# Optimization experiments

Measured on AMD Instinct MI355X. Metric: run time of the kernel, lower is better.

Reference implementation:

```python
import jax, jax.numpy as jnp
import numpy as np

N_NODES, N_EDGES, N_FEAT, DIM, HEADS, N_PRED, N_CLASS, N_STEPS = 10000, 160000, 64, 64, 4, 2, 16, 4


def setup_inputs() -> dict:
    key = jax.random.key(0)
    ks = jax.random.split(key, 16)
    def lin(k, fi, fo):
        return jax.random.normal(k, (fi, fo), jnp.float32) / np.sqrt(fi)
    return {
        "x": jax.random.normal(ks[0], (N_NODES, N_FEAT), jnp.float32),
        "edge_index": jax.random.randint(ks[1], (2, N_EDGES), 0, N_NODES, jnp.int64),
        "enc_W": lin(ks[2], N_FEAT, DIM), "enc_b": jnp.zeros((DIM,), jnp.float32),
        "gat_Wl": lin(ks[3], DIM, HEADS * DIM), "gat_bl": jnp.zeros((HEADS * DIM,), jnp.float32),
        "gat_Wr": lin(ks[4], DIM, HEADS * DIM), "gat_br": jnp.zeros((HEADS * DIM,), jnp.float32),
        "gat_att": jax.random.normal(ks[5], (HEADS, DIM), jnp.float32) / np.sqrt(DIM),
        "gat_bias": jnp.zeros((HEADS * DIM,), jnp.float32),
        "W1": lin(ks[6], HEADS * DIM, DIM), "b1": jnp.zeros((DIM,), jnp.float32),
        "W2": lin(ks[7], DIM, DIM), "b2": jnp.zeros((DIM,), jnp.float32),
        "act_W": lin(ks[8], DIM, 1), "act_b": jnp.zeros((1,), jnp.float32),
        "dec_W": jax.random.normal(ks[9], (N_PRED, DIM, N_CLASS), jnp.float32) / np.sqrt(DIM),
        "dec_b": jnp.zeros((N_PRED, N_CLASS), jnp.float32),
        "num_steps": N_STEPS,
    }


def reference(x, edge_index, enc_W, enc_b, gat_Wl, gat_bl, gat_Wr, gat_br,
              gat_att, gat_bias, W1, b1, W2, b2, act_W, act_b, dec_W, dec_b, num_steps):
    N = x.shape[0]
    H, C = gat_att.shape  # heads, per-head channels
    # PyG GATv2Conv adds self-loops by default
    loops = jnp.arange(N, dtype=edge_index.dtype)
    src = jnp.concatenate([edge_index[0], loops])
    dst = jnp.concatenate([edge_index[1], loops])

    h0 = x @ enc_W + enc_b  # encoder

    def step(carry, _):
        h, total, final = carry
        # GATv2: per-edge score on lin_l(src) + lin_r(dst)
        xl = (h @ gat_Wl + gat_bl).reshape(N, H, C)
        xr = (h @ gat_Wr + gat_br).reshape(N, H, C)
        e = jax.nn.leaky_relu(xl[src] + xr[dst], 0.2)          # [E, H, C]
        logits = jnp.einsum('ehc,hc->eh', e, gat_att)           # [E, H]
        m = jax.ops.segment_max(logits, dst, num_segments=N)    # segment softmax over dst
        ex = jnp.exp(logits - m[dst])
        denom = jax.ops.segment_sum(ex, dst, num_segments=N)
        alpha = ex / (denom[dst] + 1e-16)
        agg = jax.ops.segment_sum(xl[src] * alpha[:, :, None], dst, num_segments=N)
        g = agg.reshape(N, H * C) + gat_bias                    # concat heads + bias
        hn = jax.nn.relu(g @ W1 + b1) @ W2 + b2                 # process2 MLP
        # ACT halting: weighted accumulation, deltas clipped so weights sum to <= 1
        term = jax.nn.sigmoid(hn @ act_W + act_b)               # [N, 1]
        new_total = jnp.minimum(total + term, 1.0)
        delta = jnp.minimum(term, new_total - total)
        return (hn, total + delta, final + delta * hn), None

    carry0 = (h0, jnp.zeros((N, 1), x.dtype), jnp.zeros((N, h0.shape[1]), x.dtype))
    (_, _, final), _ = jax.lax.scan(step, carry0, None, length=num_steps)

    logits = jnp.einsum('nd,pdc->pnc', final, dec_W) + dec_b[:, None, :]
    return jax.nn.log_softmax(logits, axis=-1)  # [num_predictions, N, num_classes]
```

## Files before the change

kernel.cpp:

```cpp
#include <hip/hip_runtime.h>
#include <hip/hip_bf16.h>
#include <hip/hip_fp16.h>

#define N_NODES 10000
#define N_EDGES 160000
#define N_E2    (N_EDGES + N_NODES)
#define DIM     64
#define HD      256
#define N_PRED  2
#define N_CLASS 16
#define N_STEPS 4

typedef __hip_bfloat16 bf16;
__device__ __forceinline__ float b2f(bf16 v) { return __bfloat162float(v); }
__device__ __forceinline__ int clampn(int v) { return v < 0 ? 0 : (v >= N_NODES ? N_NODES - 1 : v); }

typedef _Float16 h2_t __attribute__((ext_vector_type(2)));

__device__ __forceinline__ float dot2(unsigned int a, unsigned int b, float c) {
#if __has_builtin(__builtin_amdgcn_fdot2)
    h2_t av, bv;
    __builtin_memcpy(&av, &a, 4);
    __builtin_memcpy(&bv, &b, 4);
    return __builtin_amdgcn_fdot2(av, bv, c, false);
#else
    __half2 ah = *(__half2*)&a, bh = *(__half2*)&b;
    float2 af = __half22float2(ah), bf = __half22float2(bh);
    return c + af.x * bf.x + af.y * bf.y;
#endif
}

struct ConvTable {
    const void* src[17];
    int start[18];
};

__device__ __forceinline__ float loadf(const void* p, int idx, int isbf16) {
    return isbf16 ? b2f(((const bf16*)p)[idx]) : ((const float*)p)[idx];
}

__global__ void detect_kernel(const unsigned int* __restrict__ e32,
                              const unsigned short* __restrict__ x16,
                              int* __restrict__ flags,
                              int* __restrict__ deg, int* __restrict__ cursor) {
    __shared__ int ce, cf;
    if (threadIdx.x == 0) { ce = 0; cf = 0; }
    __syncthreads();
    int le = 0;
    for (int i = threadIdx.x; i < 2048; i += 256)
        le += (e32[2 * i + 1] != 0u) ? 1 : 0;
    int lf = 0;
    for (int i = threadIdx.x; i < 1024; i += 256) {
        unsigned short u = x16[2 * i];
        int ex = (u >> 7) & 0xFF;
        lf += (u == 0 || (ex >= 114 && ex <= 141)) ? 1 : 0;
    }
    atomicAdd(&ce, le);
    atomicAdd(&cf, lf);
    for (int i = threadIdx.x; i < N_NODES; i += 256) { deg[i] = 0; cursor[i] = 0; }
    __syncthreads();
    if (threadIdx.x == 0) {
        flags[0] = (ce < 1024) ? 1 : 0;
        flags[1] = (cf >= 512) ? 1 : 0;
    }
}

struct PreArgs {
    ConvTable tab;
    const void* Wl_raw; const void* Wr_raw; const void* W1_raw; const void* W2_raw;
    const int* edges;
    int cb, pb;
};

__global__ void pre_kernel(PreArgs a, const int* __restrict__ flags,
                           float* __restrict__ xf, __half* __restrict__ wp,
                           int* __restrict__ deg) {
    const int b = blockIdx.x, t = threadIdx.x;
    const int isb = flags[1];
    if (b < a.cb) {
        int i = b * 256 + t;
        if (i >= a.tab.start[17]) return;
        int j = 0;
        #pragma unroll
        for (int k = 1; k < 17; ++k) j += (i >= a.tab.start[k]) ? 1 : 0;
        xf[i] = loadf(a.tab.src[j], i - a.tab.start[j], isb);
    } else if (b < a.cb + a.pb) {
        int i = (b - a.cb) * 256 + t;
        if (i >= 26624) return;
        const void* base; int width, loc;
        if (i < 8192)       { loc = i;         base = a.Wl_raw; width = 256; }
        else if (i < 16384) { loc = i - 8192;  base = a.Wr_raw; width = 256; }
        else if (i < 24576) { loc = i - 16384; base = a.W1_raw; width = 64; }
        else                { loc = i - 24576; base = a.W2_raw; width = 64; }
        int k2 = loc / width, c = loc % width;
        wp[2 * i]     = __float2half(loadf(base, (2 * k2) * width + c, isb));
        wp[2 * i + 1] = __float2half(loadf(base, (2 * k2 + 1) * width + c, isb));
    } else {
        int e = (b - a.cb - a.pb) * 256 + t;
        if (e >= N_E2) return;
        int i64 = flags[0];
        int dst;
        if (e < N_EDGES) dst = clampn(i64 ? a.edges[2 * (N_EDGES + e)] : a.edges[N_EDGES + e]);
        else             dst = e - N_EDGES;
        atomicAdd(&deg[dst], 1);
    }
}

__global__ void scan_kernel(const int* __restrict__ deg, int* __restrict__ off) {
    __shared__ int partial[1024];
    const int tid = threadIdx.x;
    const int per = (N_NODES + 1023) / 1024;
    int local[16];
    int base = tid * per;
    int s = 0;
    for (int i = 0; i < per; ++i) {
        int v = (base + i < N_NODES) ? deg[base + i] : 0;
        local[i] = s;
        s += v;
    }
    partial[tid] = s;
    __syncthreads();
    for (int d = 1; d < 1024; d <<= 1) {
        int t = (tid >= d) ? partial[tid - d] : 0;
        __syncthreads();
        partial[tid] += t;
        __syncthreads();
    }
    int offset = (tid > 0) ? partial[tid - 1] : 0;
    for (int i = 0; i < per; ++i)
        if (base + i < N_NODES) off[base + i] = offset + local[i];
    if (tid == 1023) off[N_NODES] = partial[1023];
}

struct SEArgs {
    const int* edges;
    const int* off;
    int* cursor;
    int* csr_src;
    const float* xf;
    int sX, sEncW, sEncB, sWl, sBl, sWr, sBr;
    __half* xlh;
    float* xr;
    float* act_tot;
    float* final_;
    int sb;
};

__global__ __launch_bounds__(256) void scatter_enc_kernel(SEArgs a, const int* __restrict__ flags) {
    const int b = blockIdx.x, t = threadIdx.x;
    if (b < a.sb) {
        int e = b * 256 + t;
        if (e >= N_E2) return;
        int i64 = flags[0];
        int src, dst;
        if (e < N_EDGES) {
            src = clampn(i64 ? a.edges[2 * e] : a.edges[e]);
            dst = clampn(i64 ? a.edges[2 * (N_EDGES + e)] : a.edges[N_EDGES + e]);
        } else { src = dst = e - N_EDGES; }
        int pos = a.off[dst] + atomicAdd(&a.cursor[dst], 1);
        a.csr_src[pos] = src;
        return;
    }
    __shared__ float xs[8][DIM];
    __shared__ float h0[8][DIM];
    const int pp = t >> 6, d = t & 63;
    const int n0 = (b - a.sb) * 8;
    const float* Xf   = a.xf + a.sX;
    const float* encW = a.xf + a.sEncW;
    const float* encB = a.xf + a.sEncB;
    const float* Wl   = a.xf + a.sWl;
    const float* bl   = a.xf + a.sBl;
    const float* Wr   = a.xf + a.sWr;
    const float* br   = a.xf + a.sBr;
    ((float*)xs)[t]       = Xf[n0 * DIM + t];
    ((float*)xs)[t + 256] = Xf[n0 * DIM + t + 256];
    a.final_[(size_t)n0 * DIM + t]       = 0.f;
    a.final_[(size_t)n0 * DIM + t + 256] = 0.f;
    if (t < 8) a.act_tot[n0 + t] = 0.f;
    __syncthreads();
    float ah0 = encB[d], ah1 = encB[d];
    for (int k = 0; k < DIM; ++k) {
        float wv = encW[k * DIM + d];
        ah0 += xs[pp][k] * wv;
        ah1 += xs[pp + 4][k] * wv;
    }
    h0[pp][d]     = ah0;
    h0[pp + 4][d] = ah1;
    __syncthreads();
    float al[8] = {0,0,0,0,0,0,0,0}, ar[8] = {0,0,0,0,0,0,0,0};
    for (int k = 0; k < DIM; ++k) {
        float wl = Wl[k * HD + t], wr = Wr[k * HD + t];
        #pragma unroll
        for (int j = 0; j < 8; ++j) { al[j] += h0[j][k] * wl; ar[j] += h0[j][k] * wr; }
    }
    float bbl = bl[t], bbr = br[t];
    #pragma unroll
    for (int j = 0; j < 8; ++j) {
        a.xlh[(size_t)(n0 + j) * HD + t] = __float2half(al[j] + bbl);
        a.xr[(size_t)(n0 + j) * HD + t] = ar[j] + bbr;
    }
}

__global__ __launch_bounds__(256) void step_kernel(
        const __half* __restrict__ xlh_in, const float* __restrict__ xr_in,
        const float* __restrict__ att, const float* __restrict__ gbias,
        const int* __restrict__ off, const int* __restrict__ csr_src,
        const __half* __restrict__ wp,
        const float* __restrict__ b1, const float* __restrict__ b2,
        const float* __restrict__ actW, const float* __restrict__ actB,
        const float* __restrict__ bl, const float* __restrict__ br,
        float* __restrict__ act_tot, float* __restrict__ final_,
        __half* __restrict__ xlh_out, float* __restrict__ xr_out, int do_proj) {
    __shared__ __align__(16) unsigned int gall_u[4][128];
    __shared__ float part[4][HD];
    __shared__ __half us_h[4][DIM];
    __shared__ float hns[4][DIM];
    __shared__ __half hns_h[4][DIM];
    __shared__ float delta[4];
    const int t = threadIdx.x, w = t >> 6, l = t & 63;
    const int pp = w, d = l;
    const int n0 = blockIdx.x * 4;
    const int n = n0 + w;

    {
        const int e0 = off[n], e1 = off[n + 1];
        const int elast = e1 - 1;
        const float4 xr4 = ((const float4*)(xr_in + (size_t)n * HD))[l];
        const float4 at4 = ((const float4*)att)[l];
        float m = -1e30f, s = 0.f;
        float4 acc = {0.f, 0.f, 0.f, 0.f};
        uint2 A[4], B[4];
        #pragma unroll
        for (int i = 0; i < 4; ++i) {
            int ee = e0 + i; ee = (ee > elast) ? elast : ee;
            A[i] = ((const uint2*)(xlh_in + (size_t)csr_src[ee] * HD))[l];
        }
        for (int base = e0; base < e1; base += 4) {
            #pragma unroll
            for (int i = 0; i < 4; ++i) {
                int ee = base + 4 + i; ee = (ee > elast) ? elast : ee;
                B[i] = ((const uint2*)(xlh_in + (size_t)csr_src[ee] * HD))[l];
            }
            #pragma unroll
            for (int i = 0; i < 4; ++i) {
                const bool valid = (base + i) < e1;
                __half2 h01 = *reinterpret_cast<__half2*>(&A[i].x);
                __half2 h23 = *reinterpret_cast<__half2*>(&A[i].y);
                float2 f01 = __half22float2(h01);
                float2 f23 = __half22float2(h23);
                float c0 = f01.x, c1 = f01.y, c2 = f23.x, c3 = f23.y;
                float z0 = c0 + xr4.x, z1 = c1 + xr4.y, z2 = c2 + xr4.z, z3 = c3 + xr4.w;
                z0 = (z0 > 0.f) ? z0 : 0.2f * z0;
                z1 = (z1 > 0.f) ? z1 : 0.2f * z1;
                z2 = (z2 > 0.f) ? z2 : 0.2f * z2;
                z3 = (z3 > 0.f) ? z3 : 0.2f * z3;
                float p = z0 * at4.x + z1 * at4.y + z2 * at4.z + z3 * at4.w;
                #pragma unroll
                for (int mo = 8; mo; mo >>= 1) p += __shfl_xor(p, mo, 64);
                p = valid ? p : -1e30f;
                float nm = fmaxf(m, p);
                float sc = __expf(m - nm);
                float wv = __expf(p - nm);
                s = s * sc + wv;
                acc.x = acc.x * sc + wv * c0;
                acc.y = acc.y * sc + wv * c1;
                acc.z = acc.z * sc + wv * c2;
                acc.w = acc.w * sc + wv * c3;
                m = nm;
            }
            #pragma unroll
            for (int i = 0; i < 4; ++i) A[i] = B[i];
        }
        const float inv = 1.f / (s + 1e-16f);
        const float4 gb4 = ((const float4*)gbias)[l];
        __half2 o01 = __floats2half2_rn(acc.x * inv + gb4.x, acc.y * inv + gb4.y);
        __half2 o23 = __floats2half2_rn(acc.z * inv + gb4.z, acc.w * inv + gb4.w);
        uint2 outv;
        outv.x = *(unsigned int*)&o01;
        outv.y = *(unsigned int*)&o23;
        ((uint2*)gall_u[w])[l] = outv;
    }
    __syncthreads();

    const unsigned int* Wlp = (const unsigned int*)wp;
    const unsigned int* Wrp = Wlp + 8192;
    const unsigned int* W1p = Wlp + 16384;
    const unsigned int* W2p = Wlp + 24576;

    {
        float acc[4] = {0.f, 0.f, 0.f, 0.f};
        for (int k2 = pp * 32; k2 < pp * 32 + 32; ++k2) {
            unsigned int w2 = W1p[k2 * 64 + d];
            #pragma unroll
            for (int j = 0; j < 4; ++j) acc[j] = dot2(gall_u[j][k2], w2, acc[j]);
        }
        #pragma unroll
        for (int j = 0; j < 4; ++j) part[j][t] = acc[j];
    }
    __syncthreads();
    {
        float v = part[pp][d] + part[pp][64 + d] + part[pp][128 + d] + part[pp][192 + d] + b1[d];
        us_h[pp][d] = __float2half(fmaxf(v, 0.f));
    }
    __syncthreads();
    {
        const unsigned int* us_u = (const unsigned int*)us_h;
        float acc[4] = {0.f, 0.f, 0.f, 0.f};
        for (int k2 = pp * 8; k2 < pp * 8 + 8; ++k2) {
            unsigned int w2 = W2p[k2 * 64 + d];
            #pragma unroll
            for (int j = 0; j < 4; ++j) acc[j] = dot2(us_u[j * 32 + k2], w2, acc[j]);
        }
        #pragma unroll
        for (int j = 0; j < 4; ++j) part[j][t] = acc[j];
    }
    __syncthreads();
    {
        float hv = part[pp][d] + part[pp][64 + d] + part[pp][128 + d] + part[pp][192 + d] + b2[d];
        hns[pp][d] = hv;
        hns_h[pp][d] = __float2half(hv);
    }
    __syncthreads();
    {
        float p = hns[pp][d] * actW[d];
        #pragma unroll
        for (int mo = 32; mo; mo >>= 1) p += __shfl_xor(p, mo, 64);
        if (d == 0) {
            float term = 1.f / (1.f + __expf(-(p + actB[0])));
            float tot = act_tot[n0 + pp];
            float nt = fminf(tot + term, 1.f);
            float dl = fminf(term, nt - tot);
            act_tot[n0 + pp] = tot + dl;
            delta[pp] = dl;
        }
    }
    __syncthreads();
    final_[(size_t)(n0 + pp) * DIM + d] += delta[pp] * hns[pp][d];

    if (do_proj) {
        const unsigned int* hn_u = (const unsigned int*)hns_h;
        float al[4] = {0.f, 0.f, 0.f, 0.f}, ar[4] = {0.f, 0.f, 0.f, 0.f};
        for (int k2 = 0; k2 < 32; ++k2) {
            unsigned int wl2 = Wlp[k2 * 256 + t];
            unsigned int wr2 = Wrp[k2 * 256 + t];
            #pragma unroll
            for (int j = 0; j < 4; ++j) {
                unsigned int hh = hn_u[j * 32 + k2];
                al[j] = dot2(hh, wl2, al[j]);
                ar[j] = dot2(hh, wr2, ar[j]);
            }
        }
        float bbl = bl[t], bbr = br[t];
        #pragma unroll
        for (int j = 0; j < 4; ++j) {
            xlh_out[(size_t)(n0 + j) * HD + t] = __float2half(al[j] + bbl);
            xr_out[(size_t)(n0 + j) * HD + t] = ar[j] + bbr;
        }
    }
}

__global__ void decoder_kernel(const float* __restrict__ final_,
                               const float* __restrict__ decW, const float* __restrict__ decB,
                               const int* __restrict__ flags, void* __restrict__ outv) {
    int id = blockIdx.x * 256 + threadIdx.x;
    if (id >= N_NODES * N_PRED * N_CLASS) return;
    int n = id >> 5, r = id & 31, p = r >> 4, c = r & 15;
    float acc = decB[p * N_CLASS + c];
    for (int dd = 0; dd < DIM; ++dd)
        acc += final_[(size_t)n * DIM + dd] * decW[(p * DIM + dd) * N_CLASS + c];
    float mx = acc;
    #pragma unroll
    for (int mo = 8; mo; mo >>= 1) mx = fmaxf(mx, __shfl_xor(mx, mo, 64));
    float ex = __expf(acc - mx);
    float ss = ex;
    #pragma unroll
    for (int mo = 8; mo; mo >>= 1) ss += __shfl_xor(ss, mo, 64);
    float ov = acc - mx - logf(ss);
    int oi = p * (N_NODES * N_CLASS) + n * N_CLASS + c;
    if (flags[1]) ((bf16*)outv)[oi] = __float2bfloat16(ov);
    else          ((float*)outv)[oi] = ov;
}

static size_t align256(size_t x) { return (x + 255) & ~size_t(255); }

extern "C" void kernel_launch(void* const* d_in, const int* in_sizes, int n_in,
                              void* d_out, int out_size, void* d_ws, size_t ws_size,
                              hipStream_t stream) {
    const int* edges = (const int*)d_in[1];

    static const int fids[17] = {0, 2, 3, 4, 5, 6, 7, 8, 9, 10, 11, 12, 13, 14, 15, 16, 17};
    ConvTable tab;
    int cum = 0;
    for (int i = 0; i < 17; ++i) {
        tab.src[i] = d_in[fids[i]];
        tab.start[i] = cum;
        cum += in_sizes[fids[i]];
    }
    tab.start[17] = cum;

    char* w = (char*)d_ws;
    size_t o = 0;
    int* flags     = (int*)(w + o); o = align256(o + 16 * sizeof(int));
    int* off       = (int*)(w + o); o = align256(o + (N_NODES + 1) * sizeof(int));
    int* deg       = (int*)(w + o); o = align256(o + N_NODES * sizeof(int));
    int* cursor    = (int*)(w + o); o = align256(o + N_NODES * sizeof(int));
    float* act_tot = (float*)(w + o); o = align256(o + N_NODES * sizeof(float));
    float* final_  = (float*)(w + o); o = align256(o + (size_t)N_NODES * DIM * sizeof(float));
    int* csr_src   = (int*)(w + o); o = align256(o + N_E2 * sizeof(int));
    float* xf      = (float*)(w + o); o = align256(o + (size_t)cum * sizeof(float));
    __half* xlh_a  = (__half*)(w + o); o = align256(o + (size_t)N_NODES * HD * sizeof(__half));
    float* xr_a    = (float*)(w + o); o = align256(o + (size_t)N_NODES * HD * sizeof(float));
    __half* xlh_b  = (__half*)(w + o); o = align256(o + (size_t)N_NODES * HD * sizeof(__half));
    float* xr_b    = (float*)(w + o); o = align256(o + (size_t)N_NODES * HD * sizeof(float));
    __half* wpack  = (__half*)(w + o); o = align256(o + 53248 * sizeof(__half));
    if (o > ws_size) return;

    const float* att  = xf + tab.start[7];
    const float* gbias= xf + tab.start[8];
    const float* b1   = xf + tab.start[10];
    const float* b2   = xf + tab.start[12];
    const float* actW = xf + tab.start[13];
    const float* actB = xf + tab.start[14];
    const float* decW = xf + tab.start[15];
    const float* decB = xf + tab.start[16];

    detect_kernel<<<1, 256, 0, stream>>>((const unsigned int*)d_in[1],
                                         (const unsigned short*)d_in[0], flags, deg, cursor);

    PreArgs pa;
    pa.tab = tab;
    pa.Wl_raw = d_in[4]; pa.Wr_raw = d_in[6]; pa.W1_raw = d_in[10]; pa.W2_raw = d_in[12];
    pa.edges = edges;
    pa.cb = (cum + 255) / 256;
    pa.pb = (26624 + 255) / 256;
    int hb = (N_E2 + 255) / 256;
    pre_kernel<<<pa.cb + pa.pb + hb, 256, 0, stream>>>(pa, flags, xf, wpack, deg);

    scan_kernel<<<1, 1024, 0, stream>>>(deg, off);

    SEArgs se;
    se.edges = edges; se.off = off; se.cursor = cursor; se.csr_src = csr_src;
    se.xf = xf;
    se.sX = tab.start[0]; se.sEncW = tab.start[1]; se.sEncB = tab.start[2];
    se.sWl = tab.start[3]; se.sBl = tab.start[4]; se.sWr = tab.start[5]; se.sBr = tab.start[6];
    se.xlh = xlh_a; se.xr = xr_a; se.act_tot = act_tot; se.final_ = final_;
    se.sb = hb;
    scatter_enc_kernel<<<hb + N_NODES / 8, 256, 0, stream>>>(se, flags);

    __half* xl_in = xlh_a;  float* xr_in = xr_a;
    __half* xl_out = xlh_b; float* xr_out = xr_b;
    for (int step = 0; step < N_STEPS; ++step) {
        step_kernel<<<N_NODES / 4, 256, 0, stream>>>(
            xl_in, xr_in, att, gbias, off, csr_src, wpack,
            b1, b2, actW, actB,
            xf + tab.start[4], xf + tab.start[6],
            act_tot, final_, xl_out, xr_out, (step < N_STEPS - 1) ? 1 : 0);
        __half* th = xl_in; xl_in = xl_out; xl_out = th;
        float* tf = xr_in; xr_in = xr_out; xr_out = tf;
    }

    int db = (N_NODES * N_PRED * N_CLASS + 255) / 256;
    decoder_kernel<<<db, 256, 0, stream>>>(final_, decW, decB, flags, d_out);
}
```

Measured before the change: 298.6 us.

## Fuse decoder into last GAT step, drop online softmax max, parallelize init

The decoder and log-softmax now run inside the final step_kernel launch on the block's four nodes held in shared memory, which removes a separate kernel and a reload of final_. The edge softmax no longer does an online running max with a rescale per edge. It subtracts the first edge's logit as a fixed offset, batches the shuffle reductions for four edges, and drops the epsilon. The deg/cursor zeroing in detect_kernel is spread over many blocks instead of one. Using a fixed offset risks overflow in exp if the logits within a node vary widely.

```diff
diff --git a/kernel.cpp b/kernel.cpp
--- a/kernel.cpp
+++ b/kernel.cpp
@@ -43,21 +43,23 @@
                               const unsigned short* __restrict__ x16,
                               int* __restrict__ flags,
                               int* __restrict__ deg, int* __restrict__ cursor) {
+    int i = blockIdx.x * 256 + threadIdx.x;
+    if (i < N_NODES) { deg[i] = 0; cursor[i] = 0; }
+    if (blockIdx.x != 0) return;
     __shared__ int ce, cf;
     if (threadIdx.x == 0) { ce = 0; cf = 0; }
     __syncthreads();
     int le = 0;
-    for (int i = threadIdx.x; i < 2048; i += 256)
-        le += (e32[2 * i + 1] != 0u) ? 1 : 0;
+    for (int k = threadIdx.x; k < 2048; k += 256)
+        le += (e32[2 * k + 1] != 0u) ? 1 : 0;
     int lf = 0;
-    for (int i = threadIdx.x; i < 1024; i += 256) {
-        unsigned short u = x16[2 * i];
+    for (int k = threadIdx.x; k < 1024; k += 256) {
+        unsigned short u = x16[2 * k];
         int ex = (u >> 7) & 0xFF;
         lf += (u == 0 || (ex >= 114 && ex <= 141)) ? 1 : 0;
     }
     atomicAdd(&ce, le);
     atomicAdd(&cf, lf);
-    for (int i = threadIdx.x; i < N_NODES; i += 256) { deg[i] = 0; cursor[i] = 0; }
     __syncthreads();
     if (threadIdx.x == 0) {
         flags[0] = (ce < 1024) ? 1 : 0;
@@ -209,8 +211,10 @@
         const float* __restrict__ b1, const float* __restrict__ b2,
         const float* __restrict__ actW, const float* __restrict__ actB,
         const float* __restrict__ bl, const float* __restrict__ br,
+        const float* __restrict__ decW, const float* __restrict__ decB,
         float* __restrict__ act_tot, float* __restrict__ final_,
-        __half* __restrict__ xlh_out, float* __restrict__ xr_out, int do_proj) {
+        __half* __restrict__ xlh_out, float* __restrict__ xr_out,
+        const int* __restrict__ flags, void* __restrict__ outv, int do_proj) {
     __shared__ __align__(16) unsigned int gall_u[4][128];
     __shared__ float part[4][HD];
     __shared__ __half us_h[4][DIM];
@@ -227,7 +231,7 @@
         const int elast = e1 - 1;
         const float4 xr4 = ((const float4*)(xr_in + (size_t)n * HD))[l];
         const float4 at4 = ((const float4*)att)[l];
-        float m = -1e30f, s = 0.f;
+        float s = 0.f, C = 0.f;
         float4 acc = {0.f, 0.f, 0.f, 0.f};
         uint2 A[4], B[4];
         #pragma unroll
@@ -241,44 +245,49 @@
                 int ee = base + 4 + i; ee = (ee > elast) ? elast : ee;
                 B[i] = ((const uint2*)(xlh_in + (size_t)csr_src[ee] * HD))[l];
             }
+            float p[4], cx[4], cy[4], cz[4], cw[4];
             #pragma unroll
             for (int i = 0; i < 4; ++i) {
-                const bool valid = (base + i) < e1;
                 __half2 h01 = *reinterpret_cast<__half2*>(&A[i].x);
                 __half2 h23 = *reinterpret_cast<__half2*>(&A[i].y);
                 float2 f01 = __half22float2(h01);
                 float2 f23 = __half22float2(h23);
-                float c0 = f01.x, c1 = f01.y, c2 = f23.x, c3 = f23.y;
-                float z0 = c0 + xr4.x, z1 = c1 + xr4.y, z2 = c2 + xr4.z, z3 = c3 + xr4.w;
+                cx[i] = f01.x; cy[i] = f01.y; cz[i] = f23.x; cw[i] = f23.y;
+                float z0 = cx[i] + xr4.x, z1 = cy[i] + xr4.y,
+                      z2 = cz[i] + xr4.z, z3 = cw[i] + xr4.w;
                 z0 = (z0 > 0.f) ? z0 : 0.2f * z0;
                 z1 = (z1 > 0.f) ? z1 : 0.2f * z1;
                 z2 = (z2 > 0.f) ? z2 : 0.2f * z2;
                 z3 = (z3 > 0.f) ? z3 : 0.2f * z3;
-                float p = z0 * at4.x + z1 * at4.y + z2 * at4.z + z3 * at4.w;
+                p[i] = z0 * at4.x + z1 * at4.y + z2 * at4.z + z3 * at4.w;
+            }
+            #pragma unroll
+            for (int mo = 8; mo; mo >>= 1) {
                 #pragma unroll
-                for (int mo = 8; mo; mo >>= 1) p += __shfl_xor(p, mo, 64);
-                p = valid ? p : -1e30f;
-                float nm = fmaxf(m, p);
-                float sc = __expf(m - nm);
-                float wv = __expf(p - nm);
-                s = s * sc + wv;
-                acc.x = acc.x * sc + wv * c0;
-                acc.y = acc.y * sc + wv * c1;
-                acc.z = acc.z * sc + wv * c2;
-                acc.w = acc.w * sc + wv * c3;
-                m = nm;
+                for (int i = 0; i < 4; ++i) p[i] += __shfl_xor(p[i], mo, 64);
             }
+            if (base == e0) C = p[0];
+            #pragma unroll
+            for (int i = 0; i < 4; ++i) {
+                const bool valid = (base + i) < e1;
+                float wv = valid ? __expf(p[i] - C) : 0.f;
+                s += wv;
+                acc.x += wv * cx[i];
+                acc.y += wv * cy[i];
+                acc.z += wv * cz[i];
+                acc.w += wv * cw[i];
+            }
             #pragma unroll
             for (int i = 0; i < 4; ++i) A[i] = B[i];
         }
-        const float inv = 1.f / (s + 1e-16f);
+        const float inv = 1.f / s;
         const float4 gb4 = ((const float4*)gbias)[l];
         __half2 o01 = __floats2half2_rn(acc.x * inv + gb4.x, acc.y * inv + gb4.y);
         __half2 o23 = __floats2half2_rn(acc.z * inv + gb4.z, acc.w * inv + gb4.w);
-        uint2 outv;
-        outv.x = *(unsigned int*)&o01;
-        outv.y = *(unsigned int*)&o23;
-        ((uint2*)gall_u[w])[l] = outv;
+        uint2 outv2;
+        outv2.x = *(unsigned int*)&o01;
+        outv2.y = *(unsigned int*)&o23;
+        ((uint2*)gall_u[w])[l] = outv2;
     }
     __syncthreads();
 
@@ -335,9 +344,10 @@
         }
     }
     __syncthreads();
-    final_[(size_t)(n0 + pp) * DIM + d] += delta[pp] * hns[pp][d];
+    float fnew = final_[(size_t)(n0 + pp) * DIM + d] + delta[pp] * hns[pp][d];
 
     if (do_proj) {
+        final_[(size_t)(n0 + pp) * DIM + d] = fnew;
         const unsigned int* hn_u = (const unsigned int*)hns_h;
         float al[4] = {0.f, 0.f, 0.f, 0.f}, ar[4] = {0.f, 0.f, 0.f, 0.f};
         for (int k2 = 0; k2 < 32; ++k2) {
@@ -356,29 +366,29 @@
             xlh_out[(size_t)(n0 + j) * HD + t] = __float2half(al[j] + bbl);
             xr_out[(size_t)(n0 + j) * HD + t] = ar[j] + bbr;
         }
-    }
-}
-
-__global__ void decoder_kernel(const float* __restrict__ final_,
-                               const float* __restrict__ decW, const float* __restrict__ decB,
-                               const int* __restrict__ flags, void* __restrict__ outv) {
-    int id = blockIdx.x * 256 + threadIdx.x;
-    if (id >= N_NODES * N_PRED * N_CLASS) return;
-    int n = id >> 5, r = id & 31, p = r >> 4, c = r & 15;
-    float acc = decB[p * N_CLASS + c];
-    for (int dd = 0; dd < DIM; ++dd)
-        acc += final_[(size_t)n * DIM + dd] * decW[(p * DIM + dd) * N_CLASS + c];
-    float mx = acc;
-    #pragma unroll
-    for (int mo = 8; mo; mo >>= 1) mx = fmaxf(mx, __shfl_xor(mx, mo, 64));
-    float ex = __expf(acc - mx);
-    float ss = ex;
-    #pragma unroll
-    for (int mo = 8; mo; mo >>= 1) ss += __shfl_xor(ss, mo, 64);
-    float ov = acc - mx - logf(ss);
-    int oi = p * (N_NODES * N_CLASS) + n * N_CLASS + c;
-    if (flags[1]) ((bf16*)outv)[oi] = __float2bfloat16(ov);
-    else          ((float*)outv)[oi] = ov;
+    } else {
+        float* fdec = (float*)part;
+        fdec[pp * DIM + d] = fnew;
+        __syncthreads();
+        if (t < 128) {
+            int nl = t >> 5, r = t & 31, p = r >> 4, c = r & 15;
+            float acc = decB[p * N_CLASS + c];
+            for (int dd = 0; dd < DIM; ++dd)
+                acc += fdec[nl * DIM + dd] * decW[(p * DIM + dd) * N_CLASS + c];
+            float mx = acc;
+            #pragma unroll
+            for (int mo = 8; mo; mo >>= 1) mx = fmaxf(mx, __shfl_xor(mx, mo, 64));
+            float ex = __expf(acc - mx);
+            float ss = ex;
+            #pragma unroll
+            for (int mo = 8; mo; mo >>= 1) ss += __shfl_xor(ss, mo, 64);
+            float ov = acc - mx - logf(ss);
+            int nn = n0 + nl;
+            int oi = p * (N_NODES * N_CLASS) + nn * N_CLASS + c;
+            if (flags[1]) ((bf16*)outv)[oi] = __float2bfloat16(ov);
+            else          ((float*)outv)[oi] = ov;
+        }
+    }
 }
 
 static size_t align256(size_t x) { return (x + 255) & ~size_t(255); }
@@ -424,8 +434,8 @@
     const float* decW = xf + tab.start[15];
     const float* decB = xf + tab.start[16];
 
-    detect_kernel<<<1, 256, 0, stream>>>((const unsigned int*)d_in[1],
-                                         (const unsigned short*)d_in[0], flags, deg, cursor);
+    detect_kernel<<<(N_NODES + 255) / 256, 256, 0, stream>>>(
+        (const unsigned int*)d_in[1], (const unsigned short*)d_in[0], flags, deg, cursor);
 
     PreArgs pa;
     pa.tab = tab;
@@ -454,11 +464,10 @@
             xl_in, xr_in, att, gbias, off, csr_src, wpack,
             b1, b2, actW, actB,
             xf + tab.start[4], xf + tab.start[6],
-            act_tot, final_, xl_out, xr_out, (step < N_STEPS - 1) ? 1 : 0);
+            decW, decB,
+            act_tot, final_, xl_out, xr_out,
+            flags, d_out, (step < N_STEPS - 1) ? 1 : 0);
         __half* th = xl_in; xl_in = xl_out; xl_out = th;
         float* tf = xr_in; xr_in = xr_out; xr_out = tf;
     }
-
-    int db = (N_NODES * N_PRED * N_CLASS + 255) / 256;
-    decoder_kernel<<<db, 256, 0, stream>>>(final_, decW, decB, flags, d_out);
-}
+}
```

Result: no change. 301.3 us (+0.9%).
